# Kernel optimization log

Hardware: AMD Instinct MI355X
Metric: run time of the kernel (lower is better)

The kernel has to match this reference:

```python
import jax, jax.numpy as jnp
import numpy as np
import math

B, L, DIM, H = 1, 2048, 512, 8
D = DIM // H
STEPS = 1024
TWO_PI = 2.0 * math.pi
CHUNK = 64  # matches torch chunk_size


def setup_inputs() -> dict:
    key = jax.random.key(0)
    ks = jax.random.split(key, 6)
    x = jax.random.normal(ks[0], (B, L, DIM), jnp.float32)
    W_qs = jax.random.normal(ks[1], (DIM, 2 * DIM), jnp.float32) * 0.02
    b_qs = jnp.zeros((2 * DIM,), jnp.float32)
    ln_w = jnp.ones((2 * DIM,), jnp.float32)
    ln_b = jnp.zeros((2 * DIM,), jnp.float32)
    freq = jax.random.normal(ks[2], (H,), jnp.float32) * 0.02
    phase_shift = jax.random.normal(ks[3], (H,), jnp.float32) * 0.02
    W_out = jax.random.normal(ks[4], (DIM, DIM), jnp.float32) * 0.02
    b_out = jnp.zeros((DIM,), jnp.float32)
    # buffer: cos(linspace(0, 2pi, 1024)) exactly as in _init_lookup_tables
    cos_table = jnp.cos(jnp.linspace(0.0, TWO_PI, STEPS)).astype(jnp.float32)
    return dict(x=x, W_qs=W_qs, b_qs=b_qs, ln_w=ln_w, ln_b=ln_b,
                freq=freq, phase_shift=phase_shift, W_out=W_out, b_out=b_out,
                cos_table=cos_table)


def _forward(x, W_qs, b_qs, ln_w, ln_b, freq, phase_shift, W_out, b_out, cos_table):
    # quantum state preparation (shared module applied to same x => q == k states)
    qs = x @ W_qs + b_qs                                  # [B,L,2*DIM]
    mu = jnp.mean(qs, axis=-1, keepdims=True)
    var = jnp.var(qs, axis=-1, keepdims=True)
    qs = (qs - mu) / jnp.sqrt(var + 1e-5) * ln_w + ln_b    # LayerNorm(2*dim)
    amp, phase = jnp.split(qs, 2, axis=-1)                 # [B,L,DIM] each
    amp = jax.nn.sigmoid(amp)
    amp = amp / (jnp.sqrt(jnp.sum(amp ** 2, axis=-1, keepdims=True)) + 1e-8)
    phase = jnp.tanh(phase) * math.pi

    to_heads = lambda t: t.reshape(B, L, H, D).transpose(0, 2, 1, 3)  # [B,H,L,D]
    q_amp = to_heads(amp)
    q_phase = to_heads(phase)
    v = to_heads(x)

    NC = L // CHUNK
    qa_c = q_amp.reshape(B, H, NC, CHUNK, D).transpose(2, 0, 1, 3, 4)   # [NC,B,H,C,D]
    qp_c = q_phase.reshape(B, H, NC, CHUNK, D).transpose(2, 0, 1, 3, 4)
    f = freq[None, :, None, None, None]
    s = phase_shift[None, :, None, None, None]

    def chunk(carry, qc):
        qa, qp = qc                                         # [B,H,C,D]
        # pairwise per-dim phase interference via lookup table
        pd = (qp[:, :, :, None, :] - q_phase[:, :, None, :, :]) * f + s  # [B,H,C,L,D]
        idx = ((pd / TWO_PI * STEPS) % STEPS).astype(jnp.int32)
        interf = cos_table[idx]
        score = jnp.sum(qa[:, :, :, None, :] * q_amp[:, :, None, :, :] * interf,
                        axis=-1)                            # [B,H,C,L]
        return carry, score

    _, scores = jax.lax.scan(jax.checkpoint(chunk), 0, (qa_c, qp_c))
    scores = scores.transpose(1, 2, 0, 3, 4).reshape(B, H, L, L)
    attn = jax.nn.softmax(scores / math.sqrt(D), axis=-1)
    out = jnp.einsum('bhqk,bhkd->bhqd', attn, v)            # [B,H,L,D]
    out = out.transpose(0, 2, 1, 3).reshape(B, L, DIM)
    return out @ W_out + b_out


def reference(x, W_qs, b_qs, ln_w, ln_b, freq, phase_shift, W_out, b_out, cos_table):
    return _forward(x, W_qs, b_qs, ln_w, ln_b, freq, phase_shift, W_out, b_out, cos_table)
```

## Files before the change

### kernel.cpp

```cpp
#include <hip/hip_runtime.h>
#include <cstdint>
#include <cstddef>


typedef __attribute__((ext_vector_type(8))) short short8;
typedef __attribute__((ext_vector_type(4))) float f32x4;

#define MFMA16(a, b, c) __builtin_amdgcn_mfma_f32_16x16x32_bf16((a), (b), (c), 0, 0, 0)

static constexpr size_t B_QS   = 0;
static constexpr size_t B_OP   = 0;
static constexpr size_t B_DP   = (size_t)8 * 1024 * 1024;
static constexpr size_t B_UB   = B_DP + 256 * 1024;
static constexpr size_t B_WB   = B_UB + (size_t)4 * 1024 * 1024;
static constexpr size_t B_XB   = B_WB + (size_t)4 * 1024 * 1024;
static constexpr size_t B_VT   = B_XB + (size_t)2 * 1024 * 1024;
static constexpr size_t B_WQT  = B_VT + (size_t)2 * 1024 * 1024;
static constexpr size_t B_WOT  = B_WQT + (size_t)1 * 1024 * 1024;

__device__ __forceinline__ unsigned short f2bf(float f) {
  unsigned u = __float_as_uint(f);
  return (unsigned short)((u + 0x7FFFu + ((u >> 16) & 1u)) >> 16);
}

__global__ __launch_bounds__(256) void k_prep(const float* __restrict__ x,
    const float* __restrict__ Wq, const float* __restrict__ Wo,
    unsigned short* __restrict__ xb, unsigned short* __restrict__ vT,
    unsigned short* __restrict__ WqT, unsigned short* __restrict__ WoT) {
  __shared__ float tl[64 * 65];
  const int t = threadIdx.x;
  const int b = blockIdx.x;
  if (b < 256) {
    const int i0 = (b >> 3) * 64, h = b & 7;
    #pragma unroll
    for (int it = 0; it < 16; ++it) {
      int n = t + 256 * it;
      int r = n >> 6, c = n & 63;
      float v = x[(size_t)(i0 + r) * 512 + h * 64 + c];
      tl[r * 65 + c] = v;
      xb[(size_t)(i0 + r) * 512 + h * 64 + c] = f2bf(v);
    }
    __syncthreads();
    #pragma unroll
    for (int it = 0; it < 16; ++it) {
      int n = t + 256 * it;
      int d = n >> 6, ii = n & 63;
      vT[(size_t)(h * 64 + d) * 2048 + i0 + ii] = f2bf(tl[ii * 65 + d]);
    }
  } else {
    int bb = b - 256;
    const float* src; unsigned short* dst; int k0, n0, N;
    if (bb < 128) { src = Wq; dst = WqT; k0 = (bb >> 4) * 64; n0 = (bb & 15) * 64; N = 1024; }
    else { bb -= 128; src = Wo; dst = WoT; k0 = (bb >> 3) * 64; n0 = (bb & 7) * 64; N = 512; }
    #pragma unroll
    for (int it = 0; it < 16; ++it) {
      int n = t + 256 * it;
      int r = n >> 6, c = n & 63;
      tl[r * 65 + c] = src[(size_t)(k0 + r) * N + n0 + c];
    }
    __syncthreads();
    #pragma unroll
    for (int it = 0; it < 16; ++it) {
      int n = t + 256 * it;
      int rr = n >> 6, cc = n & 63;
      dst[(size_t)(n0 + rr) * 512 + k0 + cc] = f2bf(tl[cc * 65 + rr]);
    }
  }
}

__global__ __launch_bounds__(256) void k_gemm(const unsigned short* __restrict__ A,
    const unsigned short* __restrict__ Bt, const float* __restrict__ bias,
    float* __restrict__ C, int N) {
  __shared__ __align__(16) unsigned char sm[2 * 64 * 136];
  unsigned char* s_a = sm;
  unsigned char* s_b = sm + 64 * 136;
  const int m0 = blockIdx.x * 64, n0 = blockIdx.y * 64;
  const int t = threadIdx.x;
  const int wave = t >> 6, lane = t & 63;
  const int m = lane & 15, quad = lane >> 4;
  const int sr = t >> 2, spart = t & 3;
  f32x4 acc[4] = {{0,0,0,0},{0,0,0,0},{0,0,0,0},{0,0,0,0}};
  for (int kc = 0; kc < 512; kc += 64) {
    #pragma unroll
    for (int it = 0; it < 2; ++it) {
      *(short8*)(s_a + sr * 136 + spart * 32 + it * 16) =
        *(const short8*)(A + (size_t)(m0 + sr) * 512 + kc + spart * 16 + it * 8);
      *(short8*)(s_b + sr * 136 + spart * 32 + it * 16) =
        *(const short8*)(Bt + (size_t)(n0 + sr) * 512 + kc + spart * 16 + it * 8);
    }
    __syncthreads();
    #pragma unroll
    for (int k2 = 0; k2 < 2; ++k2) {
      short8 af = *(const short8*)(s_a + (wave * 16 + m) * 136 + k2 * 64 + quad * 16);
      #pragma unroll
      for (int nt = 0; nt < 4; ++nt) {
        short8 bf = *(const short8*)(s_b + (nt * 16 + m) * 136 + k2 * 64 + quad * 16);
        acc[nt] = MFMA16(af, bf, acc[nt]);
      }
    }
    __syncthreads();
  }
  #pragma unroll
  for (int nt = 0; nt < 4; ++nt) {
    int col = n0 + nt * 16 + m;
    float bv = bias[col];
    #pragma unroll
    for (int r = 0; r < 4; ++r) {
      int row = m0 + wave * 16 + quad * 4 + r;
      C[(size_t)row * N + col] = acc[nt][r] + bv;
    }
  }
}

__global__ __launch_bounds__(256) void k_ln_act(const float* __restrict__ qs,
    const float* __restrict__ lnw, const float* __restrict__ lnb,
    const float* __restrict__ fr, const float* __restrict__ psh,
    unsigned short* __restrict__ Ub, unsigned short* __restrict__ Wb) {
  __shared__ float sred[12];
  const int i = blockIdx.x, t = threadIdx.x;
  const int wave = t >> 6, lane = t & 63;
  const float* row = qs + (size_t)i * 1024;
  float v0 = row[t], v1 = row[t + 256], v2 = row[t + 512], v3 = row[t + 768];
  float s = v0 + v1 + v2 + v3;
  float s2 = v0 * v0 + v1 * v1 + v2 * v2 + v3 * v3;
  #pragma unroll
  for (int off = 32; off; off >>= 1) {
    s += __shfl_down(s, off, 64);
    s2 += __shfl_down(s2, off, 64);
  }
  if (lane == 0) { sred[wave] = s; sred[4 + wave] = s2; }
  __syncthreads();
  s = sred[0] + sred[1] + sred[2] + sred[3];
  s2 = sred[4] + sred[5] + sred[6] + sred[7];
  float mu = s * (1.0f / 1024.0f);
  float var = s2 * (1.0f / 1024.0f) - mu * mu;
  float rstd = 1.0f / sqrtf(var + 1e-5f);
  float y0 = (v0 - mu) * rstd * lnw[t]       + lnb[t];
  float y1 = (v1 - mu) * rstd * lnw[t + 256] + lnb[t + 256];
  float y2 = (v2 - mu) * rstd * lnw[t + 512] + lnb[t + 512];
  float y3 = (v3 - mu) * rstd * lnw[t + 768] + lnb[t + 768];
  float a0 = __builtin_amdgcn_rcpf(1.0f + __expf(-y0));
  float a1 = __builtin_amdgcn_rcpf(1.0f + __expf(-y1));
  float na = a0 * a0 + a1 * a1;
  #pragma unroll
  for (int off = 32; off; off >>= 1) na += __shfl_down(na, off, 64);
  __syncthreads();
  if (lane == 0) sred[8 + wave] = na;
  __syncthreads();
  na = sred[8] + sred[9] + sred[10] + sred[11];
  float inv = 1.0f / (sqrtf(na) + 1e-8f);
  float af0 = a0 * inv, af1 = a1 * inv;
  const float PI_F = 3.14159265358979323846f;
  float e2a = __expf(2.0f * y2);
  float e2b = __expf(2.0f * y3);
  float p2 = (1.0f - 2.0f * __builtin_amdgcn_rcpf(e2a + 1.0f)) * PI_F;
  float p3 = (1.0f - 2.0f * __builtin_amdgcn_rcpf(e2b + 1.0f)) * PI_F;
  const double GAM = 1024.0 / 1023.0;
  int h0 = t >> 6, d0 = t & 63, h1 = h0 + 4;
  float c10 = (float)((double)fr[h0] * GAM);
  float s10 = (float)((double)psh[h0] * GAM);
  float c11 = (float)((double)fr[h1] * GAM);
  float s11 = (float)((double)psh[h1] * GAM);
  float A0 = fmaf(p2, c10, s10), Bp0 = p2 * c10;
  float A1 = fmaf(p3, c11, s11), Bp1 = p3 * c11;
  float cA0, sA0, cB0, sB0, cA1, sA1, cB1, sB1;
  __sincosf(A0, &sA0, &cA0);
  __sincosf(Bp0, &sB0, &cB0);
  __sincosf(A1, &sA1, &cA1);
  __sincosf(Bp1, &sB1, &cB1);
  size_t b0 = ((size_t)h0 * 2048 + i) * 128 + d0;
  size_t b1 = ((size_t)h1 * 2048 + i) * 128 + d0;
  Ub[b0] = f2bf(af0 * cA0);  Ub[b0 + 64] = f2bf(af0 * sA0);
  Wb[b0] = f2bf(af0 * cB0);  Wb[b0 + 64] = f2bf(af0 * sB0);
  Ub[b1] = f2bf(af1 * cA1);  Ub[b1 + 64] = f2bf(af1 * sA1);
  Wb[b1] = f2bf(af1 * cB1);  Wb[b1 + 64] = f2bf(af1 * sB1);
}

__global__ __launch_bounds__(256, 2) void k_flash4(const unsigned short* __restrict__ Ub,
    const unsigned short* __restrict__ Wb, const unsigned short* __restrict__ vT,
    float* __restrict__ Opart, float* __restrict__ Dpart) {
  __shared__ __align__(16) unsigned char s_w[2][64 * 272];
  __shared__ __align__(16) unsigned char s_v[2][64 * 144];
  __shared__ __align__(16) unsigned char s_p[4][16 * 144];
  const int qt = blockIdx.x, h = blockIdx.y, ks = blockIdx.z;
  const int q0 = qt * 64;
  const int t = threadIdx.x;
  const int wave = t >> 6, lane = t & 63;
  const int m = lane & 15, quad = lane >> 4;
  const int sr = t >> 2, spart = t & 3;
  unsigned char* s_pw = s_p[wave];
  short8 afr[4];
  const unsigned short* urow = Ub + ((size_t)h * 2048 + q0 + wave * 16 + m) * 128;
  #pragma unroll
  for (int fs = 0; fs < 4; ++fs)
    afr[fs] = *(const short8*)(urow + fs * 32 + quad * 8);
  short8 ones;
  #pragma unroll
  for (int j = 0; j < 8; ++j) ones[j] = (short)0x3F80;
  f32x4 oacc[4] = {{0,0,0,0},{0,0,0,0},{0,0,0,0},{0,0,0,0}};
  f32x4 dacc = {0, 0, 0, 0};
  const unsigned short* wgbase = Wb + ((size_t)h * 2048 + ks * 1024) * 128 + (size_t)sr * 128;
  const unsigned short* vgbase = vT + ((size_t)h * 64 + sr) * 2048 + ks * 1024;
  #pragma unroll
  for (int it = 0; it < 4; ++it)
    *(short8*)(s_w[0] + sr * 272 + spart * 64 + it * 16) =
      *(const short8*)(wgbase + spart * 32 + it * 8);
  #pragma unroll
  for (int it = 0; it < 2; ++it)
    *(short8*)(s_v[0] + sr * 144 + spart * 32 + it * 16) =
      *(const short8*)(vgbase + spart * 16 + it * 8);
  __syncthreads();
  for (int kt = 0; kt < 16; ++kt) {
    const int cur = kt & 1;
    short8 wst[4], vst[2];
    const bool has = (kt < 15);
    if (has) {
      const unsigned short* wg = wgbase + (size_t)(kt + 1) * 64 * 128;
      #pragma unroll
      for (int it = 0; it < 4; ++it)
        wst[it] = *(const short8*)(wg + spart * 32 + it * 8);
      const unsigned short* vg = vgbase + (kt + 1) * 64;
      #pragma unroll
      for (int it = 0; it < 2; ++it)
        vst[it] = *(const short8*)(vg + spart * 16 + it * 8);
    }
    f32x4 sc[4] = {{0,0,0,0},{0,0,0,0},{0,0,0,0},{0,0,0,0}};
    #pragma unroll
    for (int ksub = 0; ksub < 4; ++ksub)
      #pragma unroll
      for (int fs = 0; fs < 4; ++fs) {
        short8 bfr = *(const short8*)(s_w[cur] + (ksub * 16 + m) * 272 + fs * 64 + quad * 16);
        sc[ksub] = MFMA16(afr[fs], bfr, sc[ksub]);
      }
    #pragma unroll
    for (int ksub = 0; ksub < 4; ++ksub)
      #pragma unroll
      for (int r = 0; r < 4; ++r) {
        float p = __expf(sc[ksub][r] * 0.125f);
        *(unsigned short*)(s_pw + (quad * 4 + r) * 144 + (ksub * 16 + m) * 2) = f2bf(p);
      }
    if (has) {
      #pragma unroll
      for (int it = 0; it < 4; ++it)
        *(short8*)(s_w[cur ^ 1] + sr * 272 + spart * 64 + it * 16) = wst[it];
      #pragma unroll
      for (int it = 0; it < 2; ++it)
        *(short8*)(s_v[cur ^ 1] + sr * 144 + spart * 32 + it * 16) = vst[it];
    }
    __syncthreads();
    #pragma unroll
    for (int k2 = 0; k2 < 2; ++k2) {
      short8 pf = *(const short8*)(s_pw + m * 144 + k2 * 64 + quad * 16);
      dacc = MFMA16(pf, ones, dacc);
      #pragma unroll
      for (int dt = 0; dt < 4; ++dt) {
        short8 vf = *(const short8*)(s_v[cur] + (dt * 16 + m) * 144 + k2 * 64 + quad * 16);
        oacc[dt] = MFMA16(pf, vf, oacc[dt]);
      }
    }
    __syncthreads();
  }
  const size_t obase = (((size_t)ks * 8 + h) * 2048 + q0 + wave * 16) * 64;
  #pragma unroll
  for (int dt = 0; dt < 4; ++dt)
    #pragma unroll
    for (int r = 0; r < 4; ++r)
      Opart[obase + (size_t)(quad * 4 + r) * 64 + dt * 16 + m] = oacc[dt][r];
  if (m == 0) {
    #pragma unroll
    for (int r = 0; r < 4; ++r)
      Dpart[((size_t)ks * 8 + h) * 2048 + q0 + wave * 16 + quad * 4 + r] = dacc[r];
  }
}

__global__ __launch_bounds__(256) void k_out_gemm(const float* __restrict__ Opart,
    const float* __restrict__ Dpart, const unsigned short* __restrict__ WoT,
    const float* __restrict__ bo, float* __restrict__ out) {
  __shared__ __align__(16) unsigned char sm[2 * 64 * 136];
  unsigned char* s_a = sm;
  unsigned char* s_b = sm + 64 * 136;
  const int m0 = blockIdx.x * 64, n0 = blockIdx.y * 64;
  const int t = threadIdx.x;
  const int wave = t >> 6, lane = t & 63;
  const int m = lane & 15, quad = lane >> 4;
  const int sr = t >> 2, spart = t & 3;
  f32x4 acc[4] = {{0,0,0,0},{0,0,0,0},{0,0,0,0},{0,0,0,0}};
  for (int kc = 0; kc < 512; kc += 64) {
    const int h = kc >> 6;
    const int row = m0 + sr;
    float invd = 1.0f / (Dpart[(size_t)h * 2048 + row] +
                         Dpart[(size_t)(8 + h) * 2048 + row]);
    const float* o0 = Opart + ((size_t)h * 2048 + row) * 64 + spart * 16;
    const float* o1 = Opart + ((size_t)(8 + h) * 2048 + row) * 64 + spart * 16;
    unsigned short ab[16];
    #pragma unroll
    for (int it = 0; it < 4; ++it) {
      f32x4 a0 = *(const f32x4*)(o0 + it * 4);
      f32x4 a1 = *(const f32x4*)(o1 + it * 4);
      #pragma unroll
      for (int j = 0; j < 4; ++j)
        ab[it * 4 + j] = f2bf((a0[j] + a1[j]) * invd);
    }
    *(short8*)(s_a + sr * 136 + spart * 32)      = *(short8*)(ab);
    *(short8*)(s_a + sr * 136 + spart * 32 + 16) = *(short8*)(ab + 8);
    #pragma unroll
    for (int it = 0; it < 2; ++it)
      *(short8*)(s_b + sr * 136 + spart * 32 + it * 16) =
        *(const short8*)(WoT + (size_t)(n0 + sr) * 512 + kc + spart * 16 + it * 8);
    __syncthreads();
    #pragma unroll
    for (int k2 = 0; k2 < 2; ++k2) {
      short8 af = *(const short8*)(s_a + (wave * 16 + m) * 136 + k2 * 64 + quad * 16);
      #pragma unroll
      for (int nt = 0; nt < 4; ++nt) {
        short8 bf = *(const short8*)(s_b + (nt * 16 + m) * 136 + k2 * 64 + quad * 16);
        acc[nt] = MFMA16(af, bf, acc[nt]);
      }
    }
    __syncthreads();
  }
  #pragma unroll
  for (int nt = 0; nt < 4; ++nt) {
    int col = n0 + nt * 16 + m;
    float bv = bo[col];
    #pragma unroll
    for (int r = 0; r < 4; ++r) {
      int row = m0 + wave * 16 + quad * 4 + r;
      out[(size_t)row * 512 + col] = acc[nt][r] + bv;
    }
  }
}

extern "C" void kernel_launch(void* const* d_in, const int* in_sizes, int n_in,
                              void* d_out, int out_size, void* d_ws, size_t ws_size,
                              hipStream_t stream) {
  (void)in_sizes; (void)n_in; (void)out_size; (void)ws_size;
  const float* x   = (const float*)d_in[0];
  const float* Wq  = (const float*)d_in[1];
  const float* bq  = (const float*)d_in[2];
  const float* lnw = (const float*)d_in[3];
  const float* lnb = (const float*)d_in[4];
  const float* fr  = (const float*)d_in[5];
  const float* ps  = (const float*)d_in[6];
  const float* Wo  = (const float*)d_in[7];
  const float* bo  = (const float*)d_in[8];
  char* ws = (char*)d_ws;
  float*          qs    = (float*)(ws + B_QS);
  float*          Opart = (float*)(ws + B_OP);
  float*          Dpart = (float*)(ws + B_DP);
  unsigned short* Ub    = (unsigned short*)(ws + B_UB);
  unsigned short* Wb    = (unsigned short*)(ws + B_WB);
  unsigned short* xb    = (unsigned short*)(ws + B_XB);
  unsigned short* vT    = (unsigned short*)(ws + B_VT);
  unsigned short* WqT   = (unsigned short*)(ws + B_WQT);
  unsigned short* WoT   = (unsigned short*)(ws + B_WOT);
  float* out = (float*)d_out;

  k_prep<<<448, 256, 0, stream>>>(x, Wq, Wo, xb, vT, WqT, WoT);
  k_gemm<<<dim3(32, 16), 256, 0, stream>>>(xb, WqT, bq, qs, 1024);
  k_ln_act<<<2048, 256, 0, stream>>>(qs, lnw, lnb, fr, ps, Ub, Wb);
  k_flash4<<<dim3(32, 8, 2), 256, 0, stream>>>(Ub, Wb, vT, Opart, Dpart);
  k_out_gemm<<<dim3(32, 8), 256, 0, stream>>>(Opart, Dpart, WoT, bo, out);
}
```

Before: 160.6 us.

## Split keys across waves within a block and reduce partials in shared memory

The flash kernel now uses 512 threads per block, with two groups of four waves each covering half of every 128-key tile. This replaces the two-block key split that wrote fp32 partial outputs and denominators to global memory. The two halves are combined in shared memory and the normalized bf16 attention output is written directly. The existing k_gemm then does the output projection, so the separate k_out_gemm, which re-read the fp32 partials, is removed. In exchange the flash grid drops to 256 blocks, and each block needs more LDS, which could limit occupancy.

```diff
diff --git a/kernel.cpp b/kernel.cpp
--- a/kernel.cpp
+++ b/kernel.cpp
@@ -9,9 +9,8 @@
 #define MFMA16(a, b, c) __builtin_amdgcn_mfma_f32_16x16x32_bf16((a), (b), (c), 0, 0, 0)
 
 static constexpr size_t B_QS   = 0;
-static constexpr size_t B_OP   = 0;
-static constexpr size_t B_DP   = (size_t)8 * 1024 * 1024;
-static constexpr size_t B_UB   = B_DP + 256 * 1024;
+static constexpr size_t B_ATTB = 0;
+static constexpr size_t B_UB   = (size_t)8 * 1024 * 1024;
 static constexpr size_t B_WB   = B_UB + (size_t)4 * 1024 * 1024;
 static constexpr size_t B_XB   = B_WB + (size_t)4 * 1024 * 1024;
 static constexpr size_t B_VT   = B_XB + (size_t)2 * 1024 * 1024;
@@ -176,21 +175,23 @@
   Wb[b1] = f2bf(af1 * cB1);  Wb[b1 + 64] = f2bf(af1 * sB1);
 }
 
-__global__ __launch_bounds__(256, 2) void k_flash4(const unsigned short* __restrict__ Ub,
+__global__ __launch_bounds__(512, 2) void k_flash5(const unsigned short* __restrict__ Ub,
     const unsigned short* __restrict__ Wb, const unsigned short* __restrict__ vT,
-    float* __restrict__ Opart, float* __restrict__ Dpart) {
-  __shared__ __align__(16) unsigned char s_w[2][64 * 272];
-  __shared__ __align__(16) unsigned char s_v[2][64 * 144];
-  __shared__ __align__(16) unsigned char s_p[4][16 * 144];
-  const int qt = blockIdx.x, h = blockIdx.y, ks = blockIdx.z;
+    unsigned short* __restrict__ attb) {
+  __shared__ __align__(16) unsigned char s_w[2][128 * 272];
+  __shared__ __align__(16) unsigned char s_v[2][64 * 272];
+  __shared__ __align__(16) unsigned char s_p[8][16 * 144];
+  const int qt = blockIdx.x, h = blockIdx.y;
   const int q0 = qt * 64;
   const int t = threadIdx.x;
   const int wave = t >> 6, lane = t & 63;
+  const int qw = wave & 3, kw = wave >> 2;
   const int m = lane & 15, quad = lane >> 4;
-  const int sr = t >> 2, spart = t & 3;
+  const int sr = t >> 2, sp = t & 3;
+  const int vr = t >> 3, vp = t & 7;
   unsigned char* s_pw = s_p[wave];
   short8 afr[4];
-  const unsigned short* urow = Ub + ((size_t)h * 2048 + q0 + wave * 16 + m) * 128;
+  const unsigned short* urow = Ub + ((size_t)h * 2048 + q0 + qw * 16 + m) * 128;
   #pragma unroll
   for (int fs = 0; fs < 4; ++fs)
     afr[fs] = *(const short8*)(urow + fs * 32 + quad * 8);
@@ -199,39 +200,41 @@
   for (int j = 0; j < 8; ++j) ones[j] = (short)0x3F80;
   f32x4 oacc[4] = {{0,0,0,0},{0,0,0,0},{0,0,0,0},{0,0,0,0}};
   f32x4 dacc = {0, 0, 0, 0};
-  const unsigned short* wgbase = Wb + ((size_t)h * 2048 + ks * 1024) * 128 + (size_t)sr * 128;
-  const unsigned short* vgbase = vT + ((size_t)h * 64 + sr) * 2048 + ks * 1024;
+  const unsigned short* wgbase = Wb + (size_t)h * 2048 * 128 + (size_t)sr * 128;
+  const unsigned short* vgbase = vT + ((size_t)h * 64 + vr) * 2048;
   #pragma unroll
   for (int it = 0; it < 4; ++it)
-    *(short8*)(s_w[0] + sr * 272 + spart * 64 + it * 16) =
-      *(const short8*)(wgbase + spart * 32 + it * 8);
+    *(short8*)(s_w[0] + sr * 272 + sp * 64 + it * 16) =
+      *(const short8*)(wgbase + sp * 32 + it * 8);
   #pragma unroll
   for (int it = 0; it < 2; ++it)
-    *(short8*)(s_v[0] + sr * 144 + spart * 32 + it * 16) =
-      *(const short8*)(vgbase + spart * 16 + it * 8);
+    *(short8*)(s_v[0] + vr * 272 + vp * 32 + it * 16) =
+      *(const short8*)(vgbase + vp * 16 + it * 8);
   __syncthreads();
   for (int kt = 0; kt < 16; ++kt) {
     const int cur = kt & 1;
     short8 wst[4], vst[2];
     const bool has = (kt < 15);
     if (has) {
-      const unsigned short* wg = wgbase + (size_t)(kt + 1) * 64 * 128;
+      const unsigned short* wg = wgbase + (size_t)(kt + 1) * 128 * 128;
       #pragma unroll
       for (int it = 0; it < 4; ++it)
-        wst[it] = *(const short8*)(wg + spart * 32 + it * 8);
-      const unsigned short* vg = vgbase + (kt + 1) * 64;
+        wst[it] = *(const short8*)(wg + sp * 32 + it * 8);
+      const unsigned short* vg = vgbase + (kt + 1) * 128;
       #pragma unroll
       for (int it = 0; it < 2; ++it)
-        vst[it] = *(const short8*)(vg + spart * 16 + it * 8);
+        vst[it] = *(const short8*)(vg + vp * 16 + it * 8);
     }
     f32x4 sc[4] = {{0,0,0,0},{0,0,0,0},{0,0,0,0},{0,0,0,0}};
     #pragma unroll
-    for (int ksub = 0; ksub < 4; ++ksub)
+    for (int ksub = 0; ksub < 4; ++ksub) {
+      const int krow = kw * 64 + ksub * 16 + m;
       #pragma unroll
       for (int fs = 0; fs < 4; ++fs) {
-        short8 bfr = *(const short8*)(s_w[cur] + (ksub * 16 + m) * 272 + fs * 64 + quad * 16);
+        short8 bfr = *(const short8*)(s_w[cur] + krow * 272 + fs * 64 + quad * 16);
         sc[ksub] = MFMA16(afr[fs], bfr, sc[ksub]);
       }
+    }
     #pragma unroll
     for (int ksub = 0; ksub < 4; ++ksub)
       #pragma unroll
@@ -242,10 +245,10 @@
     if (has) {
       #pragma unroll
       for (int it = 0; it < 4; ++it)
-        *(short8*)(s_w[cur ^ 1] + sr * 272 + spart * 64 + it * 16) = wst[it];
+        *(short8*)(s_w[cur ^ 1] + sr * 272 + sp * 64 + it * 16) = wst[it];
       #pragma unroll
       for (int it = 0; it < 2; ++it)
-        *(short8*)(s_v[cur ^ 1] + sr * 144 + spart * 32 + it * 16) = vst[it];
+        *(short8*)(s_v[cur ^ 1] + vr * 272 + vp * 32 + it * 16) = vst[it];
     }
     __syncthreads();
     #pragma unroll
@@ -254,80 +257,41 @@
       dacc = MFMA16(pf, ones, dacc);
       #pragma unroll
       for (int dt = 0; dt < 4; ++dt) {
-        short8 vf = *(const short8*)(s_v[cur] + (dt * 16 + m) * 144 + k2 * 64 + quad * 16);
+        short8 vf = *(const short8*)(s_v[cur] + (dt * 16 + m) * 272 +
+                                     kw * 128 + k2 * 64 + quad * 16);
         oacc[dt] = MFMA16(pf, vf, oacc[dt]);
       }
     }
     __syncthreads();
   }
-  const size_t obase = (((size_t)ks * 8 + h) * 2048 + q0 + wave * 16) * 64;
-  #pragma unroll
-  for (int dt = 0; dt < 4; ++dt)
+  float* s_ored = (float*)(s_w[0]);
+  float* s_dred = (float*)(s_w[0] + 16384);
+  if (kw == 1) {
+    #pragma unroll
+    for (int dt = 0; dt < 4; ++dt)
+      #pragma unroll
+      for (int r = 0; r < 4; ++r)
+        s_ored[qw * 1024 + (quad * 4 + r) * 64 + dt * 16 + m] = oacc[dt][r];
+    if (m == 0) {
+      #pragma unroll
+      for (int r = 0; r < 4; ++r)
+        s_dred[qw * 16 + quad * 4 + r] = dacc[r];
+    }
+  }
+  __syncthreads();
+  if (kw == 0) {
+    float invd[4];
     #pragma unroll
     for (int r = 0; r < 4; ++r)
-      Opart[obase + (size_t)(quad * 4 + r) * 64 + dt * 16 + m] = oacc[dt][r];
-  if (m == 0) {
-    #pragma unroll
-    for (int r = 0; r < 4; ++r)
-      Dpart[((size_t)ks * 8 + h) * 2048 + q0 + wave * 16 + quad * 4 + r] = dacc[r];
-  }
-}
-
-__global__ __launch_bounds__(256) void k_out_gemm(const float* __restrict__ Opart,
-    const float* __restrict__ Dpart, const unsigned short* __restrict__ WoT,
-    const float* __restrict__ bo, float* __restrict__ out) {
-  __shared__ __align__(16) unsigned char sm[2 * 64 * 136];
-  unsigned char* s_a = sm;
-  unsigned char* s_b = sm + 64 * 136;
-  const int m0 = blockIdx.x * 64, n0 = blockIdx.y * 64;
-  const int t = threadIdx.x;
-  const int wave = t >> 6, lane = t & 63;
-  const int m = lane & 15, quad = lane >> 4;
-  const int sr = t >> 2, spart = t & 3;
-  f32x4 acc[4] = {{0,0,0,0},{0,0,0,0},{0,0,0,0},{0,0,0,0}};
-  for (int kc = 0; kc < 512; kc += 64) {
-    const int h = kc >> 6;
-    const int row = m0 + sr;
-    float invd = 1.0f / (Dpart[(size_t)h * 2048 + row] +
-                         Dpart[(size_t)(8 + h) * 2048 + row]);
-    const float* o0 = Opart + ((size_t)h * 2048 + row) * 64 + spart * 16;
-    const float* o1 = Opart + ((size_t)(8 + h) * 2048 + row) * 64 + spart * 16;
-    unsigned short ab[16];
-    #pragma unroll
-    for (int it = 0; it < 4; ++it) {
-      f32x4 a0 = *(const f32x4*)(o0 + it * 4);
-      f32x4 a1 = *(const f32x4*)(o1 + it * 4);
-      #pragma unroll
-      for (int j = 0; j < 4; ++j)
-        ab[it * 4 + j] = f2bf((a0[j] + a1[j]) * invd);
-    }
-    *(short8*)(s_a + sr * 136 + spart * 32)      = *(short8*)(ab);
-    *(short8*)(s_a + sr * 136 + spart * 32 + 16) = *(short8*)(ab + 8);
-    #pragma unroll
-    for (int it = 0; it < 2; ++it)
-      *(short8*)(s_b + sr * 136 + spart * 32 + it * 16) =
-        *(const short8*)(WoT + (size_t)(n0 + sr) * 512 + kc + spart * 16 + it * 8);
-    __syncthreads();
-    #pragma unroll
-    for (int k2 = 0; k2 < 2; ++k2) {
-      short8 af = *(const short8*)(s_a + (wave * 16 + m) * 136 + k2 * 64 + quad * 16);
-      #pragma unroll
-      for (int nt = 0; nt < 4; ++nt) {
-        short8 bf = *(const short8*)(s_b + (nt * 16 + m) * 136 + k2 * 64 + quad * 16);
-        acc[nt] = MFMA16(af, bf, acc[nt]);
-      }
-    }
-    __syncthreads();
-  }
-  #pragma unroll
-  for (int nt = 0; nt < 4; ++nt) {
-    int col = n0 + nt * 16 + m;
-    float bv = bo[col];
-    #pragma unroll
-    for (int r = 0; r < 4; ++r) {
-      int row = m0 + wave * 16 + quad * 4 + r;
-      out[(size_t)row * 512 + col] = acc[nt][r] + bv;
-    }
+      invd[r] = 1.0f / (dacc[r] + s_dred[qw * 16 + quad * 4 + r]);
+    #pragma unroll
+    for (int dt = 0; dt < 4; ++dt)
+      #pragma unroll
+      for (int r = 0; r < 4; ++r) {
+        float o = oacc[dt][r] + s_ored[qw * 1024 + (quad * 4 + r) * 64 + dt * 16 + m];
+        attb[(size_t)(q0 + qw * 16 + quad * 4 + r) * 512 + h * 64 + dt * 16 + m] =
+            f2bf(o * invd[r]);
+      }
   }
 }
 
@@ -345,20 +309,19 @@
   const float* Wo  = (const float*)d_in[7];
   const float* bo  = (const float*)d_in[8];
   char* ws = (char*)d_ws;
-  float*          qs    = (float*)(ws + B_QS);
-  float*          Opart = (float*)(ws + B_OP);
-  float*          Dpart = (float*)(ws + B_DP);
-  unsigned short* Ub    = (unsigned short*)(ws + B_UB);
-  unsigned short* Wb    = (unsigned short*)(ws + B_WB);
-  unsigned short* xb    = (unsigned short*)(ws + B_XB);
-  unsigned short* vT    = (unsigned short*)(ws + B_VT);
-  unsigned short* WqT   = (unsigned short*)(ws + B_WQT);
-  unsigned short* WoT   = (unsigned short*)(ws + B_WOT);
+  float*          qs   = (float*)(ws + B_QS);
+  unsigned short* attb = (unsigned short*)(ws + B_ATTB);
+  unsigned short* Ub   = (unsigned short*)(ws + B_UB);
+  unsigned short* Wb   = (unsigned short*)(ws + B_WB);
+  unsigned short* xb   = (unsigned short*)(ws + B_XB);
+  unsigned short* vT   = (unsigned short*)(ws + B_VT);
+  unsigned short* WqT  = (unsigned short*)(ws + B_WQT);
+  unsigned short* WoT  = (unsigned short*)(ws + B_WOT);
   float* out = (float*)d_out;
 
   k_prep<<<448, 256, 0, stream>>>(x, Wq, Wo, xb, vT, WqT, WoT);
   k_gemm<<<dim3(32, 16), 256, 0, stream>>>(xb, WqT, bq, qs, 1024);
   k_ln_act<<<2048, 256, 0, stream>>>(qs, lnw, lnb, fr, ps, Ub, Wb);
-  k_flash4<<<dim3(32, 8, 2), 256, 0, stream>>>(Ub, Wb, vT, Opart, Dpart);
-  k_out_gemm<<<dim3(32, 8), 256, 0, stream>>>(Opart, Dpart, WoT, bo, out);
-}
+  k_flash5<<<dim3(32, 8), 512, 0, stream>>>(Ub, Wb, vT, attb);
+  k_gemm<<<dim3(32, 8), 256, 0, stream>>>(attb, WoT, bo, out, 512);
+}
```

Result: faster. 156.0 us (-2.9%).
